# Kernel tuning notes

Hardware: AMD Instinct MI355X
Metric: run time of the kernel (lower is better)

## Reference

```python
import jax, jax.numpy as jnp
import numpy as np

# ---- db6 filter bank (pywt conventions) ----
_REC_LO = np.array([0.11154074335008017, 0.4946238903983854, 0.7511339080215775,
                    0.3152503517092432, -0.22626469396516913, -0.12976686756709563,
                    0.09750160558707936, 0.02752286553001629, -0.031582039318031156,
                    0.0005538422009938016, 0.004777257511010651, -0.00107730108499558],
                   dtype=np.float32)
_REC_HI = _REC_LO[::-1].copy(); _REC_HI[1::2] *= -1.0          # qmf(rec_lo)
_DEC_LO = _REC_LO[::-1].copy()
_DEC_HI = _REC_HI[::-1].copy()
L = 12          # filter length
LEVEL = 8       # J
# pytorch_wavelets cross-correlates with dec[::-1] == true conv with dec.
# lax.conv_general_dilated is correlation, so analysis kernels = dec[::-1] = rec filters.
ANA = jnp.asarray(np.stack([_REC_LO, _REC_HI])[:, None, :])     # [2,1,L]
SYN = jnp.asarray(np.stack([_DEC_LO, _DEC_HI])[None, :, :])     # [1,2,L]


def dwt1d(x, J):
    """Multi-level DWT, mode='symmetric'. x: [B,C,N] -> (yl [B,C,m], [yh1..yhJ])."""
    B, C, N = x.shape
    lo = x.reshape(B * C, 1, N)
    highs = []
    for _ in range(J):
        n = lo.shape[-1]
        outlen = (n + L - 1) // 2                    # pywt dwt_coeff_len
        p = 2 * (outlen - 1) - n + L
        xp = jnp.pad(lo, ((0, 0), (0, 0), (p // 2, (p + 1) // 2)), mode='symmetric')
        y = jax.lax.conv_general_dilated(xp, ANA, (2,), 'VALID',
                                         dimension_numbers=('NCH', 'OIH', 'NCH'))
        lo = y[:, :1]
        highs.append(y[:, 1:].reshape(B, C, outlen))
    return lo.reshape(B, C, -1), highs


def idwt1d(yl, yhs):
    """Inverse of dwt1d. yl: [B,C,m], yhs list (level1..levelJ)."""
    B, C, _ = yl.shape
    lo = yl.reshape(B * C, 1, -1)
    pad = L - 1 - (L - 2)                            # torch convT padding L-2 -> lax pad 1
    for h in yhs[::-1]:
        h = h.reshape(B * C, 1, -1)
        if lo.shape[-1] > h.shape[-1]:               # 'unpad' extra sample
            lo = lo[..., :h.shape[-1]]
        xh = jnp.concatenate([lo, h], axis=1)        # [BC,2,n]
        lo = jax.lax.conv_general_dilated(xh, SYN, (1,), [(pad, pad)],
                                          lhs_dilation=(2,),
                                          dimension_numbers=('NCH', 'OIH', 'NCH'))
    return lo.reshape(B, C, -1)


def wno_forward(x, fc0_w, fc0_b, w1, w2, cw, cb, fc1_w, fc1_b, fc2_w, fc2_b):
    B, s, _ = x.shape
    grid = jnp.broadcast_to(jnp.linspace(0.0, 1.0, s, dtype=x.dtype)[None, :, None], (B, s, 1))
    v = jnp.concatenate([x, grid], axis=-1) @ fc0_w + fc0_b     # [B,s,W]
    v = v.transpose(0, 2, 1)                                     # [B,W,s]
    n_layers = w1.shape[0]
    for i in range(n_layers):
        yl, yhs = dwt1d(v, LEVEL)
        yl = jnp.einsum('bix,iox->box', yl, w1[i])               # mix approx coeffs
        yhs[-1] = jnp.einsum('bix,iox->box', yhs[-1], w2[i])     # mix finest-level detail
        x1 = idwt1d(yl, yhs)
        x2 = jnp.einsum('bis,io->bos', v, cw[i]) + cb[i][None, :, None]  # 1x1 conv
        v = x1 + x2
        if i < n_layers - 1:
            v = jax.nn.gelu(v, approximate=False)
    v = v.transpose(0, 2, 1)
    v = jax.nn.gelu(v @ fc1_w + fc1_b, approximate=False)
    return v @ fc2_w + fc2_b                                     # [B,s,1]


def setup_inputs() -> dict:
    key = jax.random.key(0)
    B, S, W, NL = 32, 8192, 64, 4
    n = S
    for _ in range(LEVEL):
        n = (n + L - 1) // 2
    modes = n                                                    # 42
    ks = jax.random.split(key, 12)
    scale = 1.0 / (W * W)
    return {
        'x': jax.random.normal(ks[0], (B, S, 1), jnp.float32),
        'fc0_w': jax.random.normal(ks[1], (2, W), jnp.float32) * 0.5,
        'fc0_b': jax.random.normal(ks[2], (W,), jnp.float32) * 0.1,
        'w1': scale * jax.random.uniform(ks[3], (NL, W, W, modes), jnp.float32),
        'w2': scale * jax.random.uniform(ks[4], (NL, W, W, modes), jnp.float32),
        'cw': jax.random.normal(ks[5], (NL, W, W), jnp.float32) * (1.0 / np.sqrt(W)),
        'cb': jax.random.normal(ks[6], (NL, W), jnp.float32) * 0.05,
        'fc1_w': jax.random.normal(ks[7], (W, 128), jnp.float32) * (1.0 / np.sqrt(W)),
        'fc1_b': jax.random.normal(ks[8], (128,), jnp.float32) * 0.05,
        'fc2_w': jax.random.normal(ks[9], (128, 1), jnp.float32) * (1.0 / np.sqrt(128.0)),
        'fc2_b': jax.random.normal(ks[10], (1,), jnp.float32) * 0.05,
    }


def reference(x, fc0_w, fc0_b, w1, w2, cw, cb, fc1_w, fc1_b, fc2_w, fc2_b):
    return wno_forward(x, fc0_w, fc0_b, w1, w2, cw, cb, fc1_w, fc1_b, fc2_w, fc2_b)
```

## Files before the change

kernel.cpp:

```cpp
#include <hip/hip_runtime.h>
#include <cmath>

#define BC 2048
#define S_LEN 8192
#define MODES 42
#define HTOT 8232

static constexpr float C_LO[12] = {
  0.11154074335008017f, 0.4946238903983854f, 0.7511339080215775f,
  0.3152503517092432f, -0.22626469396516913f, -0.12976686756709563f,
  0.09750160558707936f, 0.02752286553001629f, -0.031582039318031156f,
  0.0005538422009938016f, 0.004777257511010651f, -0.00107730108499558f };

__device__ __forceinline__ float rec_lo_c(int k){ return C_LO[k]; }
__device__ __forceinline__ float rec_hi_c(int k){ float v = C_LO[11-k]; return (k&1)? -v : v; }
__device__ __forceinline__ float dec_lo_c(int k){ return C_LO[11-k]; }
__device__ __forceinline__ float dec_hi_c(int k){ float v = C_LO[k];    return (k&1)?  v : -v; }

__device__ __forceinline__ float gelu_f(float x){
  return 0.5f * x * (1.0f + erff(x * 0.70710678118654752440f));
}

__device__ __forceinline__ int reflect_i(int t, int n){
  t = (t < 0) ? (-1 - t) : t;
  t = (t >= n) ? (2 * n - 1 - t) : t;
  return t;
}

__device__ __forceinline__ unsigned short bf16_rn(float x){
  unsigned int b = __float_as_uint(x);
  b += 0x7FFF + ((b >> 16) & 1);
  return (unsigned short)(b >> 16);
}
__device__ __forceinline__ float bf16_to_f(unsigned short h){
  return __uint_as_float(((unsigned int)h) << 16);
}

typedef short  v8s __attribute__((ext_vector_type(8)));
typedef float  v4f __attribute__((ext_vector_type(4)));

__global__ __launch_bounds__(256) void fc0_kernel(
    const float* __restrict__ x, const float* __restrict__ w,
    const float* __restrict__ bias, float* __restrict__ v)
{
  int p = blockIdx.x * 256 + threadIdx.x;
  int b = p >> 13, s = p & 8191;
  float xv = x[p];
  float g  = (float)s * (1.0f / 8191.0f);
  for (int c = 0; c < 64; ++c) {
    v[((size_t)(b * 64 + c)) * S_LEN + s] = xv * w[c] + g * w[64 + c] + bias[c];
  }
}

__global__ __launch_bounds__(256) void dwt_big(
    const float* __restrict__ vin, float* __restrict__ highs, float* __restrict__ lo_f)
{
  __shared__ float sV[2184], sL1[1088], sL2[544];
  int seq = blockIdx.x >> 2, c = blockIdx.x & 3;
  const float* src = vin + (size_t)seq * S_LEN;
  float* hseq = highs + (size_t)seq * HTOT;

  int V0 = 2080 * c - 70;
  for (int i = threadIdx.x; i < 2178; i += 256)
    sV[i] = src[reflect_i(V0 + i, 8192)];
  __syncthreads();

  int base1 = 1040 * c - 30;
  for (int u = threadIdx.x; u < 1082; u += 256) {
    int m1 = base1 + u;
    float alo = 0.f, ahi = 0.f;
    #pragma unroll
    for (int k = 0; k < 12; ++k) {
      float x = sV[2 * m1 + k - 10 - V0];
      alo += x * rec_lo_c(k); ahi += x * rec_hi_c(k);
    }
    sL1[u] = alo;
    if (m1 >= 1040 * c && m1 < 1040 * c + 1040 && m1 >= 0 && m1 < 4101) hseq[m1] = ahi;
  }
  __syncthreads();

  int base2 = 520 * c - 10;
  for (int u = threadIdx.x; u < 534; u += 256) {
    int m2 = base2 + u;
    float alo = 0.f, ahi = 0.f;
    #pragma unroll
    for (int k = 0; k < 12; ++k) {
      int t = reflect_i(2 * m2 + k - 10, 4101);
      float x = sL1[t - base1];
      alo += x * rec_lo_c(k); ahi += x * rec_hi_c(k);
    }
    sL2[u] = alo;
    if (m2 >= 520 * c && m2 < 520 * c + 520 && m2 >= 0 && m2 < 2056) hseq[4101 + m2] = ahi;
  }
  __syncthreads();

  for (int u = threadIdx.x; u < 260; u += 256) {
    int m3 = 260 * c + u;
    if (m3 < 1033) {
      float alo = 0.f, ahi = 0.f;
      #pragma unroll
      for (int k = 0; k < 12; ++k) {
        int t = reflect_i(2 * m3 + k - 10, 2056);
        float x = sL2[t - base2];
        alo += x * rec_lo_c(k); ahi += x * rec_hi_c(k);
      }
      lo_f[(size_t)seq * 1033 + m3] = alo;
      hseq[6157 + m3] = ahi;
    }
  }
}

__device__ __forceinline__ void dwt_lvl(const float* in, int n, float* out, int outn, float* hg)
{
  for (int m = threadIdx.x; m < outn; m += 256) {
    float alo = 0.f, ahi = 0.f;
    #pragma unroll
    for (int k = 0; k < 12; ++k) {
      float x = in[reflect_i(2 * m + k - 10, n)];
      alo += x * rec_lo_c(k); ahi += x * rec_hi_c(k);
    }
    out[m] = alo; hg[m] = ahi;
  }
  __syncthreads();
}

__global__ __launch_bounds__(256) void dwt_small(
    const float* __restrict__ lo_f, float* __restrict__ highs, float* __restrict__ yl)
{
  __shared__ float A[1040], Bb[528];
  int seq = blockIdx.x;
  const float* src = lo_f + (size_t)seq * 1033;
  float* hseq = highs + (size_t)seq * HTOT;
  for (int i = threadIdx.x; i < 1033; i += 256) A[i] = src[i];
  __syncthreads();
  dwt_lvl(A, 1033, Bb, 522, hseq + 7190);
  dwt_lvl(Bb, 522, A, 266, hseq + 7712);
  dwt_lvl(A, 266, Bb, 138, hseq + 7978);
  dwt_lvl(Bb, 138, A, 74, hseq + 8116);
  dwt_lvl(A, 74, Bb, 42, hseq + 8190);
  for (int m = threadIdx.x; m < MODES; m += 256) yl[seq * MODES + m] = Bb[m];
}

__global__ __launch_bounds__(256) void mix42(
    const float* __restrict__ in, int in_stride,
    const float* __restrict__ w, float* __restrict__ out)
{
  int idx = blockIdx.x * 256 + threadIdx.x;
  if (idx >= 32 * 64 * MODES) return;
  int xx = idx % MODES;
  int o  = (idx / MODES) % 64;
  int b  = idx / (MODES * 64);
  float acc = 0.f;
  for (int i = 0; i < 64; ++i)
    acc += in[((size_t)(b * 64 + i)) * in_stride + xx] * w[(i * 64 + o) * MODES + xx];
  out[(b * 64 + o) * MODES + xx] = acc;
}

__device__ __forceinline__ void idwt_lvl(const float* lo, const float* h, float* out, int outn)
{
  const int par = threadIdx.x & 1;
  for (int m = threadIdx.x; m < outn; m += 256) {
    int t0 = (m - par) >> 1;
    float acc = 0.f;
    #pragma unroll
    for (int i = 0; i < 6; ++i) {
      float cl = par ? dec_lo_c(2 * i) : dec_lo_c(2 * i + 1);
      float ch = par ? dec_hi_c(2 * i) : dec_hi_c(2 * i + 1);
      acc += lo[t0 + i] * cl + h[t0 + i] * ch;
    }
    out[m] = acc;
  }
}

__device__ __forceinline__ void stage_band(float* dst, const float* src, int len, int alloc)
{
  for (int i = threadIdx.x; i < alloc; i += 256) dst[i] = (i < len) ? src[i] : 0.f;
}

__global__ __launch_bounds__(256) void idwt_small(
    const float* __restrict__ yl_m, const float* __restrict__ yh_m,
    const float* __restrict__ highs, float* __restrict__ lo_i)
{
  __shared__ float bands[1132];
  __shared__ float wa[1040], wb[528];
  int seq = blockIdx.x;
  const float* hseq = highs + (size_t)seq * HTOT;
  stage_band(bands + 0,   yl_m + (size_t)seq * MODES, 42, 50);
  stage_band(bands + 50,  yh_m + (size_t)seq * MODES, 42, 50);
  stage_band(bands + 100, hseq + 8116, 74, 82);
  stage_band(bands + 182, hseq + 7978, 138, 146);
  stage_band(bands + 328, hseq + 7712, 266, 274);
  stage_band(bands + 602, hseq + 7190, 522, 530);
  __syncthreads();
  idwt_lvl(bands + 0, bands + 50, wa, 74);    __syncthreads();
  idwt_lvl(wa, bands + 100, wb, 138);         __syncthreads();
  idwt_lvl(wb, bands + 182, wa, 266);         __syncthreads();
  idwt_lvl(wa, bands + 328, wb, 522);         __syncthreads();
  const int par = threadIdx.x & 1;
  for (int m = threadIdx.x; m < 1033; m += 256) {
    int t0 = (m - par) >> 1;
    float acc = 0.f;
    #pragma unroll
    for (int i = 0; i < 6; ++i) {
      float cl = par ? dec_lo_c(2 * i) : dec_lo_c(2 * i + 1);
      float ch = par ? dec_hi_c(2 * i) : dec_hi_c(2 * i + 1);
      acc += wb[t0 + i] * cl + bands[602 + t0 + i] * ch;
    }
    lo_i[(size_t)seq * 1033 + m] = acc;
  }
}

__global__ __launch_bounds__(256) void idwt_big(
    const float* __restrict__ lo_i, const float* __restrict__ highs, float* __restrict__ x1)
{
  __shared__ float sL3[280], sH3[280], sL2[544], sH2[544], sL1[1040], sH1[1040];
  int seq = blockIdx.x >> 2, c = blockIdx.x & 3;
  const float* hseq = highs + (size_t)seq * HTOT;
  const float* l3   = lo_i + (size_t)seq * 1033;
  int b3 = 256 * c - 2, b2 = 512 * c - 2, b1 = 1024 * c - 2;
  const int par = threadIdx.x & 1;

  for (int i = threadIdx.x; i < 280; i += 256) {
    int g = b3 + i;
    bool ok = (g >= 0 && g < 1033);
    sL3[i] = ok ? l3[g] : 0.f;
    sH3[i] = ok ? hseq[6157 + g] : 0.f;
  }
  for (int i = threadIdx.x; i < 536; i += 256) {
    int g = b2 + i;
    sH2[i] = (g >= 0 && g < 2056) ? hseq[4101 + g] : 0.f;
  }
  for (int i = threadIdx.x; i < 1040; i += 256) {
    int g = b1 + i;
    sH1[i] = (g >= 0 && g < 4101) ? hseq[g] : 0.f;
  }
  __syncthreads();

  for (int u = threadIdx.x; u < 536; u += 256) {
    int m = b2 + u;
    int t0 = ((m - par) >> 1) - b3;
    float acc = 0.f;
    #pragma unroll
    for (int i = 0; i < 6; ++i) {
      float cl = par ? dec_lo_c(2 * i) : dec_lo_c(2 * i + 1);
      float ch = par ? dec_hi_c(2 * i) : dec_hi_c(2 * i + 1);
      acc += sL3[t0 + i] * cl + sH3[t0 + i] * ch;
    }
    sL2[u] = (m >= 0 && m < 2056) ? acc : 0.f;
  }
  __syncthreads();

  for (int u = threadIdx.x; u < 1040; u += 256) {
    int m = b1 + u;
    int t0 = ((m - par) >> 1) - b2;
    float acc = 0.f;
    #pragma unroll
    for (int i = 0; i < 6; ++i) {
      float cl = par ? dec_lo_c(2 * i) : dec_lo_c(2 * i + 1);
      float ch = par ? dec_hi_c(2 * i) : dec_hi_c(2 * i + 1);
      acc += sL2[t0 + i] * cl + sH2[t0 + i] * ch;
    }
    sL1[u] = (m >= 0 && m < 4101) ? acc : 0.f;
  }
  __syncthreads();

  for (int u = threadIdx.x; u < 2048; u += 256) {
    int m = 2048 * c + u;
    int t0 = ((m - par) >> 1) - b1;
    float acc = 0.f;
    #pragma unroll
    for (int i = 0; i < 6; ++i) {
      float cl = par ? dec_lo_c(2 * i) : dec_lo_c(2 * i + 1);
      float ch = par ? dec_hi_c(2 * i) : dec_hi_c(2 * i + 1);
      acc += sL1[t0 + i] * cl + sH1[t0 + i] * ch;
    }
    x1[(size_t)seq * S_LEN + m] = acc;
  }
}

__global__ __launch_bounds__(256) void pw_mfma(
    const float* __restrict__ x1, float* v,
    const float* __restrict__ cw, const float* __restrict__ cb, int do_gelu)
{
  __shared__ unsigned short aH[64][64], aL[64][64];
  __shared__ unsigned short wH[64][64], wL[64][64];
  __shared__ float cbl[64];
  int b  = blockIdx.x >> 7;
  int s0 = (blockIdx.x & 127) << 6;
  int t  = threadIdx.x;

  for (int r = 0; r < 16; ++r) {
    int idx = t + 256 * r;
    int c = idx >> 6, o = idx & 63;
    float wv = cw[idx];
    unsigned short h = bf16_rn(wv);
    float lo = wv - bf16_to_f(h);
    int cs = c ^ ((o & 7) << 3);
    wH[o][cs] = h; wL[o][cs] = bf16_rn(lo);
  }
  if (t < 64) cbl[t] = cb[t];
  for (int r = 0; r < 16; ++r) {
    int idx = t + 256 * r;
    int ch = idx >> 6, p = idx & 63;
    float x = v[((size_t)(b * 64 + ch)) * S_LEN + s0 + p];
    unsigned short h = bf16_rn(x);
    float lo = x - bf16_to_f(h);
    int cs = ch ^ ((p & 7) << 3);
    aH[p][cs] = h; aL[p][cs] = bf16_rn(lo);
  }
  __syncthreads();

  int l = t & 63, wv_ = t >> 6;
  int pi = l & 15, kg = l >> 4;
  int pos = wv_ * 16 + pi;
  int swz = (pi & 7) << 3;

  v4f acc[4];
  #pragma unroll
  for (int i = 0; i < 4; ++i) acc[i] = v4f{0.f, 0.f, 0.f, 0.f};

  #pragma unroll
  for (int kt = 0; kt < 2; ++kt) {
    int ka = (kg * 8 + kt * 32) ^ swz;
    v8s ah = *(const v8s*)&aH[pos][ka];
    v8s al = *(const v8s*)&aL[pos][ka];
    #pragma unroll
    for (int ct = 0; ct < 4; ++ct) {
      int o = ct * 16 + pi;
      v8s bh = *(const v8s*)&wH[o][ka];
      v8s bl = *(const v8s*)&wL[o][ka];
      acc[ct] = __builtin_amdgcn_mfma_f32_16x16x32_bf16(ah, bh, acc[ct], 0, 0, 0);
      acc[ct] = __builtin_amdgcn_mfma_f32_16x16x32_bf16(ah, bl, acc[ct], 0, 0, 0);
      acc[ct] = __builtin_amdgcn_mfma_f32_16x16x32_bf16(al, bh, acc[ct], 0, 0, 0);
    }
  }

  #pragma unroll
  for (int ct = 0; ct < 4; ++ct) {
    int o = ct * 16 + pi;
    size_t base = ((size_t)(b * 64 + o)) * S_LEN + s0 + wv_ * 16 + kg * 4;
    float4 x4 = *(const float4*)&x1[base];
    float cbv = cbl[o];
    float y0 = acc[ct][0] + x4.x + cbv;
    float y1 = acc[ct][1] + x4.y + cbv;
    float y2 = acc[ct][2] + x4.z + cbv;
    float y3 = acc[ct][3] + x4.w + cbv;
    if (do_gelu) { y0 = gelu_f(y0); y1 = gelu_f(y1); y2 = gelu_f(y2); y3 = gelu_f(y3); }
    float4 y4 = make_float4(y0, y1, y2, y3);
    *(float4*)&v[base] = y4;
  }
}

__global__ __launch_bounds__(256) void head_mfma(
    const float* __restrict__ v, const float* __restrict__ fc1w,
    const float* __restrict__ fc1b, const float* __restrict__ fc2w,
    const float* __restrict__ fc2b, float* __restrict__ out)
{
  __shared__ unsigned short aH[64][64], aL[64][64];
  __shared__ unsigned short wH[128][64], wL[128][64];
  __shared__ float f1b[128], f2w[128];
  int b  = blockIdx.x >> 7;
  int s0 = (blockIdx.x & 127) << 6;
  int t  = threadIdx.x;

  for (int r = 0; r < 32; ++r) {
    int idx = t + 256 * r;
    int c = idx >> 7, j = idx & 127;
    float wv = fc1w[idx];
    unsigned short h = bf16_rn(wv);
    float lo = wv - bf16_to_f(h);
    int cs = c ^ ((j & 7) << 3);
    wH[j][cs] = h; wL[j][cs] = bf16_rn(lo);
  }
  if (t < 128) { f1b[t] = fc1b[t]; f2w[t] = fc2w[t]; }
  for (int r = 0; r < 16; ++r) {
    int idx = t + 256 * r;
    int ch = idx >> 6, p = idx & 63;
    float x = v[((size_t)(b * 64 + ch)) * S_LEN + s0 + p];
    unsigned short h = bf16_rn(x);
    float lo = x - bf16_to_f(h);
    int cs = ch ^ ((p & 7) << 3);
    aH[p][cs] = h; aL[p][cs] = bf16_rn(lo);
  }
  __syncthreads();

  int l = t & 63, wv_ = t >> 6;
  int pi = l & 15, kg = l >> 4;
  int pos = wv_ * 16 + pi;
  int swz = (pi & 7) << 3;

  v4f acc[8];
  #pragma unroll
  for (int i = 0; i < 8; ++i) acc[i] = v4f{0.f, 0.f, 0.f, 0.f};

  #pragma unroll
  for (int kt = 0; kt < 2; ++kt) {
    int ka = (kg * 8 + kt * 32) ^ swz;
    v8s ah = *(const v8s*)&aH[pos][ka];
    v8s al = *(const v8s*)&aL[pos][ka];
    #pragma unroll
    for (int ct = 0; ct < 8; ++ct) {
      int j = ct * 16 + pi;
      v8s bh = *(const v8s*)&wH[j][ka];
      v8s bl = *(const v8s*)&wL[j][ka];
      acc[ct] = __builtin_amdgcn_mfma_f32_16x16x32_bf16(ah, bh, acc[ct], 0, 0, 0);
      acc[ct] = __builtin_amdgcn_mfma_f32_16x16x32_bf16(ah, bl, acc[ct], 0, 0, 0);
      acc[ct] = __builtin_amdgcn_mfma_f32_16x16x32_bf16(al, bh, acc[ct], 0, 0, 0);
    }
  }

  float part[4] = {0.f, 0.f, 0.f, 0.f};
  #pragma unroll
  for (int ct = 0; ct < 8; ++ct) {
    int j = ct * 16 + pi;
    float bias = f1b[j], f2 = f2w[j];
    #pragma unroll
    for (int r = 0; r < 4; ++r) {
      float d = acc[ct][r] + bias;
      part[r] += f2 * gelu_f(d);
    }
  }
  #pragma unroll
  for (int r = 0; r < 4; ++r) {
    part[r] += __shfl_xor(part[r], 1, 16);
    part[r] += __shfl_xor(part[r], 2, 16);
    part[r] += __shfl_xor(part[r], 4, 16);
    part[r] += __shfl_xor(part[r], 8, 16);
  }
  if (pi == 0) {
    float b2 = fc2b[0];
    float4 o4 = make_float4(part[0] + b2, part[1] + b2, part[2] + b2, part[3] + b2);
    *(float4*)&out[(size_t)b * S_LEN + s0 + wv_ * 16 + kg * 4] = o4;
  }
}

extern "C" void kernel_launch(void* const* d_in, const int* in_sizes, int n_in,
                              void* d_out, int out_size, void* d_ws, size_t ws_size,
                              hipStream_t stream) {
  const float* x    = (const float*)d_in[0];
  const float* fc0w = (const float*)d_in[1];
  const float* fc0b = (const float*)d_in[2];
  const float* w1   = (const float*)d_in[3];
  const float* w2   = (const float*)d_in[4];
  const float* cw   = (const float*)d_in[5];
  const float* cb   = (const float*)d_in[6];
  const float* fc1w = (const float*)d_in[7];
  const float* fc1b = (const float*)d_in[8];
  const float* fc2w = (const float*)d_in[9];
  const float* fc2b = (const float*)d_in[10];
  float* out = (float*)d_out;

  float* ws     = (float*)d_ws;
  float* v      = ws;
  float* x1     = v      + (size_t)BC * S_LEN;
  float* highs  = x1     + (size_t)BC * S_LEN;
  float* yl_raw = highs  + (size_t)BC * HTOT;
  float* yl_m   = yl_raw + (size_t)BC * MODES;
  float* yh_m   = yl_m   + (size_t)BC * MODES;
  float* lo_f   = yh_m   + (size_t)BC * MODES;
  float* lo_i   = lo_f   + (size_t)BC * 1033;
  size_t needed = (size_t)((lo_i + (size_t)BC * 1033) - ws) * sizeof(float);
  if (ws_size < needed) return;

  fc0_kernel<<<1024, 256, 0, stream>>>(x, fc0w, fc0b, v);

  for (int i = 0; i < 4; ++i) {
    dwt_big<<<BC * 4, 256, 0, stream>>>(v, highs, lo_f);
    dwt_small<<<BC, 256, 0, stream>>>(lo_f, highs, yl_raw);
    mix42<<<336, 256, 0, stream>>>(yl_raw, MODES, w1 + (size_t)i * 64 * 64 * MODES, yl_m);
    mix42<<<336, 256, 0, stream>>>(highs + 8190, HTOT, w2 + (size_t)i * 64 * 64 * MODES, yh_m);
    idwt_small<<<BC, 256, 0, stream>>>(yl_m, yh_m, highs, lo_i);
    idwt_big<<<BC * 4, 256, 0, stream>>>(lo_i, highs, x1);
    pw_mfma<<<4096, 256, 0, stream>>>(x1, v, cw + i * 4096, cb + i * 64, (i < 3) ? 1 : 0);
  }

  head_mfma<<<4096, 256, 0, stream>>>(v, fc1w, fc1b, fc2w, fc2b, out);
}
```

Before: 680.2 us.

## Presplit weights once, vectorize activation loads, merge mix launches, use fast erf

A new prep kernel runs once per call and splits the pointwise and head weights into swizzled bf16 hi/lo arrays. The per-block weight conversion in pw_mfma and head_mfma becomes a plain vector copy. Activation tiles are now read as float4, and the two mix42 launches are merged into one kernel. GELU switches from erff to an Abramowitz-Stegun polynomial approximation with a fast exp, which saves ALU work but adds approximation error.

```diff
diff --git a/kernel.cpp b/kernel.cpp
--- a/kernel.cpp
+++ b/kernel.cpp
@@ -17,8 +17,15 @@
 __device__ __forceinline__ float dec_lo_c(int k){ return C_LO[11-k]; }
 __device__ __forceinline__ float dec_hi_c(int k){ float v = C_LO[k];    return (k&1)?  v : -v; }
 
+__device__ __forceinline__ float erf_fast(float x){
+  float ax = fabsf(x);
+  float t  = __fdividef(1.0f, 1.0f + 0.3275911f * ax);
+  float p  = ((((1.061405429f * t - 1.453152027f) * t) + 1.421413741f) * t - 0.284496736f) * t + 0.254829592f;
+  float y  = 1.0f - p * t * __expf(-ax * ax);
+  return copysignf(y, x);
+}
 __device__ __forceinline__ float gelu_f(float x){
-  return 0.5f * x * (1.0f + erff(x * 0.70710678118654752440f));
+  return 0.5f * x * (1.0f + erf_fast(x * 0.70710678118654752440f));
 }
 
 __device__ __forceinline__ int reflect_i(int t, int n){
@@ -38,6 +45,33 @@
 
 typedef short  v8s __attribute__((ext_vector_type(8)));
 typedef float  v4f __attribute__((ext_vector_type(4)));
+typedef unsigned short u16;
+
+__global__ __launch_bounds__(256) void prep_split(
+    const float* __restrict__ fc1w, const float* __restrict__ cw,
+    u16* __restrict__ whH, u16* __restrict__ whL,
+    u16* __restrict__ wcH, u16* __restrict__ wcL)
+{
+  int i = blockIdx.x * 256 + threadIdx.x;
+  if (i < 8192) {
+    int c = i >> 7, j = i & 127;
+    float wv = fc1w[i];
+    u16 h = bf16_rn(wv);
+    float lo = wv - bf16_to_f(h);
+    int cs = c ^ ((j & 7) << 3);
+    whH[j * 64 + cs] = h; whL[j * 64 + cs] = bf16_rn(lo);
+  }
+  int k = i - 8192;
+  if (k >= 0 && k < 16384) {
+    int l = k >> 12, r = k & 4095;
+    int c = r >> 6, o = r & 63;
+    float wv = cw[k];
+    u16 h = bf16_rn(wv);
+    float lo = wv - bf16_to_f(h);
+    int cs = c ^ ((o & 7) << 3);
+    wcH[l * 4096 + o * 64 + cs] = h; wcL[l * 4096 + o * 64 + cs] = bf16_rn(lo);
+  }
+}
 
 __global__ __launch_bounds__(256) void fc0_kernel(
     const float* __restrict__ x, const float* __restrict__ w,
@@ -141,19 +175,24 @@
   for (int m = threadIdx.x; m < MODES; m += 256) yl[seq * MODES + m] = Bb[m];
 }
 
-__global__ __launch_bounds__(256) void mix42(
-    const float* __restrict__ in, int in_stride,
-    const float* __restrict__ w, float* __restrict__ out)
-{
-  int idx = blockIdx.x * 256 + threadIdx.x;
+__global__ __launch_bounds__(256) void mix2(
+    const float* __restrict__ yl_raw, const float* __restrict__ highs,
+    const float* __restrict__ w1i, const float* __restrict__ w2i,
+    float* __restrict__ yl_m, float* __restrict__ yh_m)
+{
+  bool hi = blockIdx.x >= 336;
+  int idx = (blockIdx.x - (hi ? 336 : 0)) * 256 + threadIdx.x;
   if (idx >= 32 * 64 * MODES) return;
   int xx = idx % MODES;
   int o  = (idx / MODES) % 64;
   int b  = idx / (MODES * 64);
+  const float* in = hi ? (highs + 8190) : yl_raw;
+  size_t stride   = hi ? HTOT : MODES;
+  const float* w  = hi ? w2i : w1i;
   float acc = 0.f;
   for (int i = 0; i < 64; ++i)
-    acc += in[((size_t)(b * 64 + i)) * in_stride + xx] * w[(i * 64 + o) * MODES + xx];
-  out[(b * 64 + o) * MODES + xx] = acc;
+    acc += in[((size_t)(b * 64 + i)) * stride + xx] * w[(i * 64 + o) * MODES + xx];
+  (hi ? yh_m : yl_m)[(b * 64 + o) * MODES + xx] = acc;
 }
 
 __device__ __forceinline__ void idwt_lvl(const float* lo, const float* h, float* out, int outn)
@@ -280,33 +319,38 @@
 
 __global__ __launch_bounds__(256) void pw_mfma(
     const float* __restrict__ x1, float* v,
-    const float* __restrict__ cw, const float* __restrict__ cb, int do_gelu)
-{
-  __shared__ unsigned short aH[64][64], aL[64][64];
-  __shared__ unsigned short wH[64][64], wL[64][64];
+    const u16* __restrict__ wcH, const u16* __restrict__ wcL,
+    const float* __restrict__ cb, int do_gelu)
+{
+  __shared__ u16 aH[64][64], aL[64][64];
+  __shared__ u16 wH[64][64], wL[64][64];
   __shared__ float cbl[64];
   int b  = blockIdx.x >> 7;
   int s0 = (blockIdx.x & 127) << 6;
   int t  = threadIdx.x;
 
-  for (int r = 0; r < 16; ++r) {
+  {
+    const v8s* srcH = (const v8s*)wcH;
+    const v8s* srcL = (const v8s*)wcL;
+    v8s* dstH = (v8s*)&wH[0][0];
+    v8s* dstL = (v8s*)&wL[0][0];
+    #pragma unroll
+    for (int r = 0; r < 2; ++r) {
+      dstH[t + 256 * r] = srcH[t + 256 * r];
+      dstL[t + 256 * r] = srcL[t + 256 * r];
+    }
+  }
+  if (t < 64) cbl[t] = cb[t];
+
+  #pragma unroll
+  for (int r = 0; r < 4; ++r) {
     int idx = t + 256 * r;
-    int c = idx >> 6, o = idx & 63;
-    float wv = cw[idx];
-    unsigned short h = bf16_rn(wv);
-    float lo = wv - bf16_to_f(h);
-    int cs = c ^ ((o & 7) << 3);
-    wH[o][cs] = h; wL[o][cs] = bf16_rn(lo);
-  }
-  if (t < 64) cbl[t] = cb[t];
-  for (int r = 0; r < 16; ++r) {
-    int idx = t + 256 * r;
-    int ch = idx >> 6, p = idx & 63;
-    float x = v[((size_t)(b * 64 + ch)) * S_LEN + s0 + p];
-    unsigned short h = bf16_rn(x);
-    float lo = x - bf16_to_f(h);
-    int cs = ch ^ ((p & 7) << 3);
-    aH[p][cs] = h; aL[p][cs] = bf16_rn(lo);
+    int ch = idx >> 4, p4 = (idx & 15) << 2;
+    float4 xv = *(const float4*)&v[((size_t)(b * 64 + ch)) * S_LEN + s0 + p4];
+    u16 h0 = bf16_rn(xv.x); aH[p4+0][ch ^ (((p4+0)&7)<<3)] = h0; aL[p4+0][ch ^ (((p4+0)&7)<<3)] = bf16_rn(xv.x - bf16_to_f(h0));
+    u16 h1 = bf16_rn(xv.y); aH[p4+1][ch ^ (((p4+1)&7)<<3)] = h1; aL[p4+1][ch ^ (((p4+1)&7)<<3)] = bf16_rn(xv.y - bf16_to_f(h1));
+    u16 h2 = bf16_rn(xv.z); aH[p4+2][ch ^ (((p4+2)&7)<<3)] = h2; aL[p4+2][ch ^ (((p4+2)&7)<<3)] = bf16_rn(xv.z - bf16_to_f(h2));
+    u16 h3 = bf16_rn(xv.w); aH[p4+3][ch ^ (((p4+3)&7)<<3)] = h3; aL[p4+3][ch ^ (((p4+3)&7)<<3)] = bf16_rn(xv.w - bf16_to_f(h3));
   }
   __syncthreads();
 
@@ -352,35 +396,40 @@
 }
 
 __global__ __launch_bounds__(256) void head_mfma(
-    const float* __restrict__ v, const float* __restrict__ fc1w,
+    const float* __restrict__ v,
+    const u16* __restrict__ whH, const u16* __restrict__ whL,
     const float* __restrict__ fc1b, const float* __restrict__ fc2w,
     const float* __restrict__ fc2b, float* __restrict__ out)
 {
-  __shared__ unsigned short aH[64][64], aL[64][64];
-  __shared__ unsigned short wH[128][64], wL[128][64];
+  __shared__ u16 aH[64][64], aL[64][64];
+  __shared__ u16 wH[128][64], wL[128][64];
   __shared__ float f1b[128], f2w[128];
   int b  = blockIdx.x >> 7;
   int s0 = (blockIdx.x & 127) << 6;
   int t  = threadIdx.x;
 
-  for (int r = 0; r < 32; ++r) {
+  {
+    const v8s* srcH = (const v8s*)whH;
+    const v8s* srcL = (const v8s*)whL;
+    v8s* dstH = (v8s*)&wH[0][0];
+    v8s* dstL = (v8s*)&wL[0][0];
+    #pragma unroll
+    for (int r = 0; r < 4; ++r) {
+      dstH[t + 256 * r] = srcH[t + 256 * r];
+      dstL[t + 256 * r] = srcL[t + 256 * r];
+    }
+  }
+  if (t < 128) { f1b[t] = fc1b[t]; f2w[t] = fc2w[t]; }
+
+  #pragma unroll
+  for (int r = 0; r < 4; ++r) {
     int idx = t + 256 * r;
-    int c = idx >> 7, j = idx & 127;
-    float wv = fc1w[idx];
-    unsigned short h = bf16_rn(wv);
-    float lo = wv - bf16_to_f(h);
-    int cs = c ^ ((j & 7) << 3);
-    wH[j][cs] = h; wL[j][cs] = bf16_rn(lo);
-  }
-  if (t < 128) { f1b[t] = fc1b[t]; f2w[t] = fc2w[t]; }
-  for (int r = 0; r < 16; ++r) {
-    int idx = t + 256 * r;
-    int ch = idx >> 6, p = idx & 63;
-    float x = v[((size_t)(b * 64 + ch)) * S_LEN + s0 + p];
-    unsigned short h = bf16_rn(x);
-    float lo = x - bf16_to_f(h);
-    int cs = ch ^ ((p & 7) << 3);
-    aH[p][cs] = h; aL[p][cs] = bf16_rn(lo);
+    int ch = idx >> 4, p4 = (idx & 15) << 2;
+    float4 xv = *(const float4*)&v[((size_t)(b * 64 + ch)) * S_LEN + s0 + p4];
+    u16 h0 = bf16_rn(xv.x); aH[p4+0][ch ^ (((p4+0)&7)<<3)] = h0; aL[p4+0][ch ^ (((p4+0)&7)<<3)] = bf16_rn(xv.x - bf16_to_f(h0));
+    u16 h1 = bf16_rn(xv.y); aH[p4+1][ch ^ (((p4+1)&7)<<3)] = h1; aL[p4+1][ch ^ (((p4+1)&7)<<3)] = bf16_rn(xv.y - bf16_to_f(h1));
+    u16 h2 = bf16_rn(xv.z); aH[p4+2][ch ^ (((p4+2)&7)<<3)] = h2; aL[p4+2][ch ^ (((p4+2)&7)<<3)] = bf16_rn(xv.z - bf16_to_f(h2));
+    u16 h3 = bf16_rn(xv.w); aH[p4+3][ch ^ (((p4+3)&7)<<3)] = h3; aL[p4+3][ch ^ (((p4+3)&7)<<3)] = bf16_rn(xv.w - bf16_to_f(h3));
   }
   __syncthreads();
 
@@ -459,20 +508,25 @@
   float* yh_m   = yl_m   + (size_t)BC * MODES;
   float* lo_f   = yh_m   + (size_t)BC * MODES;
   float* lo_i   = lo_f   + (size_t)BC * 1033;
-  size_t needed = (size_t)((lo_i + (size_t)BC * 1033) - ws) * sizeof(float);
+  u16*   whH    = (u16*)(lo_i + (size_t)BC * 1033);
+  u16*   whL    = whH + 8192;
+  u16*   wcH    = whL + 8192;
+  u16*   wcL    = wcH + 16384;
+  size_t needed = (size_t)((char*)(wcL + 16384) - (char*)ws);
   if (ws_size < needed) return;
 
+  prep_split<<<96, 256, 0, stream>>>(fc1w, cw, whH, whL, wcH, wcL);
   fc0_kernel<<<1024, 256, 0, stream>>>(x, fc0w, fc0b, v);
 
   for (int i = 0; i < 4; ++i) {
     dwt_big<<<BC * 4, 256, 0, stream>>>(v, highs, lo_f);
     dwt_small<<<BC, 256, 0, stream>>>(lo_f, highs, yl_raw);
-    mix42<<<336, 256, 0, stream>>>(yl_raw, MODES, w1 + (size_t)i * 64 * 64 * MODES, yl_m);
-    mix42<<<336, 256, 0, stream>>>(highs + 8190, HTOT, w2 + (size_t)i * 64 * 64 * MODES, yh_m);
+    mix2<<<672, 256, 0, stream>>>(yl_raw, highs, w1 + (size_t)i * 64 * 64 * MODES,
+                                  w2 + (size_t)i * 64 * 64 * MODES, yl_m, yh_m);
     idwt_small<<<BC, 256, 0, stream>>>(yl_m, yh_m, highs, lo_i);
     idwt_big<<<BC * 4, 256, 0, stream>>>(lo_i, highs, x1);
-    pw_mfma<<<4096, 256, 0, stream>>>(x1, v, cw + i * 4096, cb + i * 64, (i < 3) ? 1 : 0);
-  }
-
-  head_mfma<<<4096, 256, 0, stream>>>(v, fc1w, fc1b, fc2w, fc2b, out);
-}
+    pw_mfma<<<4096, 256, 0, stream>>>(x1, v, wcH + i * 4096, wcL + i * 4096, cb + i * 64, (i < 3) ? 1 : 0);
+  }
+
+  head_mfma<<<4096, 256, 0, stream>>>(v, whH, whL, fc1b, fc2w, fc2b, out);
+}
```

After: 641.3 us. 5.7% less time.
